# Optimization experiments

Hardware: AMD Instinct MI355X
Metric: run time of the kernel (lower is better)

The kernel has to match this reference:

```python
import jax, jax.numpy as jnp
import numpy as np

B, Hh, Ww, C = 16, 56, 56, 256
NH, WS, SS = 8, 7, 3
HD = C // NH
N = WS * WS
SCALE = HD ** -0.5
EPS = 1e-5


def _rel_pos_index():
    coords = np.stack(np.meshgrid(np.arange(WS), np.arange(WS), indexing='ij'))  # (2, ws, ws)
    cf = coords.reshape(2, -1)
    rc = (cf[:, :, None] - cf[:, None, :]).transpose(1, 2, 0).astype(np.int64)  # (N, N, 2)
    rc[:, :, 0] += WS - 1
    rc[:, :, 1] += WS - 1
    rc[:, :, 0] *= 2 * WS - 1
    return jnp.asarray(rc.sum(-1))  # (N, N)

REL_IDX = _rel_pos_index()


def _shift_mask():
    # standard Swin SW-MSA mask for cyclic shift
    img = np.zeros((1, Hh, Ww, 1), dtype=np.float32)
    cnt = 0
    for hs in (slice(0, -WS), slice(-WS, -SS), slice(-SS, None)):
        for ws_ in (slice(0, -WS), slice(-WS, -SS), slice(-SS, None)):
            img[:, hs, ws_, :] = cnt
            cnt += 1
    mw = img.reshape(1, Hh // WS, WS, Ww // WS, WS, 1).transpose(0, 1, 3, 2, 4, 5).reshape(-1, N)
    am = mw[:, None, :] - mw[:, :, None]
    return jnp.asarray(np.where(am != 0, -100.0, 0.0).astype(np.float32))  # (nW, N, N)


def _ln(x, g, b):
    mu = x.mean(-1, keepdims=True)
    var = ((x - mu) ** 2).mean(-1, keepdims=True)
    return (x - mu) * jax.lax.rsqrt(var + EPS) * g + b


def setup_inputs() -> dict:
    key = jax.random.key(0)
    ks = jax.random.split(key, 8)
    return {
        'x': jax.random.normal(ks[0], (B, Hh * Ww, C), jnp.float32),
        'mask': _shift_mask(),
        'norm1_g': jnp.ones((C,), jnp.float32),
        'norm1_b': jnp.zeros((C,), jnp.float32),
        'qkv_w': jax.random.normal(ks[1], (3 * C, C), jnp.float32) * 0.02,
        'qkv_b': jnp.zeros((3 * C,), jnp.float32),
        'rel_bias': jax.random.normal(ks[2], ((2 * WS - 1) ** 2, NH), jnp.float32) * 0.02,
        'proj_w': jax.random.normal(ks[3], (C, C), jnp.float32) * 0.02,
        'proj_b': jnp.zeros((C,), jnp.float32),
        'norm2_g': jnp.ones((C,), jnp.float32),
        'norm2_b': jnp.zeros((C,), jnp.float32),
        'fc1_w': jax.random.normal(ks[4], (4 * C, C), jnp.float32) * 0.02,
        'fc1_b': jnp.zeros((4 * C,), jnp.float32),
        'fc2_w': jax.random.normal(ks[5], (C, 4 * C), jnp.float32) * 0.02,
        'fc2_b': jnp.zeros((C,), jnp.float32),
    }


def reference(x, mask, norm1_g, norm1_b, qkv_w, qkv_b, rel_bias, proj_w, proj_b,
              norm2_g, norm2_b, fc1_w, fc1_b, fc2_w, fc2_b):
    shortcut = x
    h = _ln(x, norm1_g, norm1_b).reshape(B, Hh, Ww, C)
    # cyclic shift
    h = jnp.roll(h, (-SS, -SS), axis=(1, 2))
    # window partition -> (B*nW, N, C)
    hw = h.reshape(B, Hh // WS, WS, Ww // WS, WS, C).transpose(0, 1, 3, 2, 4, 5).reshape(-1, N, C)
    # qkv projection
    qkv = (hw @ qkv_w.T + qkv_b).reshape(-1, N, 3, NH, HD).transpose(2, 0, 3, 1, 4)
    q, k, v = qkv[0] * SCALE, qkv[1], qkv[2]  # (Bw, NH, N, HD)
    attn = jnp.einsum('bhnd,bhmd->bhnm', q, k)  # (Bw, NH, N, N)
    rpb = rel_bias[REL_IDX.reshape(-1)].reshape(N, N, NH).transpose(2, 0, 1)
    attn = attn + rpb[None]
    nW = mask.shape[0]
    attn = attn.reshape(B, nW, NH, N, N) + mask[None, :, None]
    attn = jax.nn.softmax(attn.reshape(-1, NH, N, N), axis=-1)
    o = jnp.einsum('bhnm,bhmd->bhnd', attn, v).transpose(0, 2, 1, 3).reshape(-1, N, C)
    o = o @ proj_w.T + proj_b
    # window reverse
    o = o.reshape(B, Hh // WS, Ww // WS, WS, WS, C).transpose(0, 1, 3, 2, 4, 5).reshape(B, Hh, Ww, C)
    o = jnp.roll(o, (SS, SS), axis=(1, 2)).reshape(B, Hh * Ww, C)
    x = shortcut + o
    h2 = _ln(x, norm2_g, norm2_b)
    h2 = jax.nn.gelu(h2 @ fc1_w.T + fc1_b, approximate=False)
    return x + (h2 @ fc2_w.T + fc2_b)
```

## Files before the change

kernel.cpp:

```cpp
#include <hip/hip_runtime.h>
#include <cmath>

#define B_    16
#define HH    56
#define WWI   56
#define C_    256
#define NH_   8
#define WS_   7
#define SS_   3
#define HD_   32
#define NTOK  50176
#define NN    49
#define SCALE_ 0.17677669529663689f
#define EPS_  1e-5f

typedef __bf16  bf16x8  __attribute__((ext_vector_type(8)));
typedef float   f32x4   __attribute__((ext_vector_type(4)));
typedef unsigned short ushort8v __attribute__((ext_vector_type(8)));

__device__ __forceinline__ unsigned short f2bf(float f) {
    unsigned int u = __float_as_uint(f);
    unsigned int r = u + 0x7FFFu + ((u >> 16) & 1u);
    return (unsigned short)(r >> 16);
}
__device__ __forceinline__ float bf2f(unsigned short h) {
    return __uint_as_float(((unsigned int)h) << 16);
}
__device__ __forceinline__ float gelu_t(float x) {
    float t = 0.7978845608028654f * (x + 0.044715f * x * x * x);
    float e = __expf(2.0f * t);
    float th = 1.0f - 2.0f * __builtin_amdgcn_rcpf(e + 1.0f);
    return 0.5f * x * (1.0f + th);
}

__device__ __forceinline__ void gload_lds16(const unsigned short* g, unsigned short* l) {
    __builtin_amdgcn_global_load_lds(
        (const __attribute__((address_space(1))) unsigned int*)g,
        (__attribute__((address_space(3))) unsigned int*)l, 16, 0, 0);
}

__global__ __launch_bounds__(256) void convw_k(
    const float* __restrict__ qkvw, const float* __restrict__ projw,
    const float* __restrict__ fc1w, const float* __restrict__ fc2w,
    unsigned short* __restrict__ dst)
{
    int i = blockIdx.x * 256 + threadIdx.x;
    float v;
    if      (i < 196608) v = qkvw[i];
    else if (i < 262144) v = projw[i - 196608];
    else if (i < 524288) v = fc1w[i - 262144];
    else                 v = fc2w[i - 524288];
    dst[i] = f2bf(v);
}

__global__ __launch_bounds__(256) void cb_k(
    const float* __restrict__ mask, const float* __restrict__ relb,
    unsigned short* __restrict__ cb)
{
    int s = blockIdx.x;
    int wi = s >> 3, head = s & 7;
    for (int p = threadIdx.x; p < 2408; p += 256) {
        float v = 0.0f;
        if (p < 2401) {
            int i = p / NN, j = p - i * NN;
            int di = i / 7 - j / 7 + 6, dj = i % 7 - j % 7 + 6;
            v = relb[(di * 13 + dj) * NH_ + head] + mask[(size_t)wi * 2401 + p];
        }
        cb[(size_t)s * 2408 + p] = f2bf(v);
    }
}

__global__ __launch_bounds__(256) void ln_k(
    const float* __restrict__ x, const float* __restrict__ g,
    const float* __restrict__ bta, unsigned short* __restrict__ dst, int shifted)
{
    int wave = threadIdx.x >> 6, lane = threadIdx.x & 63;
    int tok = blockIdx.x * 4 + wave;
    const float4 v = *(const float4*)(x + (size_t)tok * C_ + lane * 4);
    float s = v.x + v.y + v.z + v.w;
    float q = v.x*v.x + v.y*v.y + v.z*v.z + v.w*v.w;
    for (int o = 32; o > 0; o >>= 1) { s += __shfl_xor(s, o, 64); q += __shfl_xor(q, o, 64); }
    float mu  = s * (1.0f / C_);
    float var = q * (1.0f / C_) - mu * mu;
    float rs  = rsqrtf(var + EPS_);
    float4 gg = *(const float4*)(g   + lane * 4);
    float4 bb = *(const float4*)(bta + lane * 4);
    float y0 = (v.x - mu) * rs * gg.x + bb.x;
    float y1 = (v.y - mu) * rs * gg.y + bb.y;
    float y2 = (v.z - mu) * rs * gg.z + bb.z;
    float y3 = (v.w - mu) * rs * gg.w + bb.w;
    size_t di;
    if (shifted) {
        int b = tok / 3136, p = tok % 3136;
        int ph = p / 56, pw = p % 56;
        int sh = ph - SS_; if (sh < 0) sh += HH;
        int sw = pw - SS_; if (sw < 0) sw += WWI;
        int bw = b * 64 + (sh / WS_) * 8 + (sw / WS_);
        int n  = (sh % WS_) * WS_ + (sw % WS_);
        di = ((size_t)bw * NN + n) * C_ + lane * 4;
    } else {
        di = (size_t)tok * C_ + lane * 4;
    }
    unsigned int lo = (unsigned int)f2bf(y0) | ((unsigned int)f2bf(y1) << 16);
    unsigned int hi = (unsigned int)f2bf(y2) | ((unsigned int)f2bf(y3) << 16);
    uint2 u; u.x = lo; u.y = hi;
    *(uint2*)(dst + di) = u;
}

template<int EPI, int NT>
__global__ __launch_bounds__(256) void gemm_k(
    const unsigned short* __restrict__ A, const unsigned short* __restrict__ Bt,
    int K, const float* __restrict__ bias,
    const float* __restrict__ resid, float* __restrict__ outF,
    unsigned short* __restrict__ outQ, unsigned short* __restrict__ outK,
    unsigned short* __restrict__ outV)
{
    __shared__ __align__(16) unsigned char smem[49152];
    const int tid = threadIdx.x;
    const int lin = blockIdx.x;
    const int xcd = lin & 7, t = lin >> 3;
    const int m0 = (xcd * 49 + t / NT) * 128;
    const int n0 = (t % NT) * 128;
    const int wave = tid >> 6, lane = tid & 63, quad = lane >> 4, l16 = lane & 15;
    const int wm = wave >> 1, wn = wave & 1;
    const int r0 = tid >> 2, c0 = (tid & 3) * 8;

    const size_t gA0 = (size_t)(m0 + r0) * K + c0;
    const size_t gA1 = (size_t)(m0 + r0 + 64) * K + c0;
    const size_t gB0 = (size_t)(n0 + r0) * K + c0;
    const size_t gB1 = (size_t)(n0 + r0 + 64) * K + c0;
    const int woff = wave * 512;

    f32x4 acc[4][4] = {};
    const int nk = K >> 5;
    #pragma unroll
    for (int p = 0; p < 2; ++p) {
        unsigned short* sA = (unsigned short*)(smem + p * 16384);
        unsigned short* sB = sA + 4096;
        const int kp = p << 5;
        gload_lds16(A + gA0 + kp, sA + woff);
        gload_lds16(A + gA1 + kp, sA + woff + 2048);
        gload_lds16(Bt + gB0 + kp, sB + woff);
        gload_lds16(Bt + gB1 + kp, sB + woff + 2048);
    }
    int bufc = 0;
    for (int kk = 0; kk < nk; ++kk) {
        if (kk + 2 < nk) {
            int bufn = bufc + 2; if (bufn >= 3) bufn -= 3;
            unsigned short* sA = (unsigned short*)(smem + bufn * 16384);
            unsigned short* sB = sA + 4096;
            const int k2 = (kk + 2) << 5;
            gload_lds16(A + gA0 + k2, sA + woff);
            gload_lds16(A + gA1 + k2, sA + woff + 2048);
            gload_lds16(Bt + gB0 + k2, sB + woff);
            gload_lds16(Bt + gB1 + k2, sB + woff + 2048);
            __asm volatile("s_waitcnt vmcnt(8)\n\ts_barrier" ::: "memory");
        } else if (kk + 1 < nk) {
            __asm volatile("s_waitcnt vmcnt(4)\n\ts_barrier" ::: "memory");
        } else {
            __asm volatile("s_waitcnt vmcnt(0)\n\ts_barrier" ::: "memory");
        }
        const unsigned short* sA = (const unsigned short*)(smem + bufc * 16384);
        const unsigned short* sB = sA + 4096;
        bf16x8 af[4], bfr[4];
        #pragma unroll
        for (int tt = 0; tt < 4; ++tt) {
            af[tt]  = __builtin_bit_cast(bf16x8, *(const ushort8v*)(sA + (wm * 64 + tt * 16 + l16) * 32 + quad * 8));
            bfr[tt] = __builtin_bit_cast(bf16x8, *(const ushort8v*)(sB + (wn * 64 + tt * 16 + l16) * 32 + quad * 8));
        }
        #pragma unroll
        for (int mt = 0; mt < 4; ++mt)
            #pragma unroll
            for (int nt = 0; nt < 4; ++nt)
                acc[mt][nt] = __builtin_amdgcn_mfma_f32_16x16x32_bf16(af[mt], bfr[nt], acc[mt][nt], 0, 0, 0);
        __asm volatile("s_barrier" ::: "memory");
        if (++bufc == 3) bufc = 0;
    }

    float b4[4];
    #pragma unroll
    for (int nt = 0; nt < 4; ++nt) b4[nt] = bias[n0 + wn * 64 + nt * 16 + l16];

    if (EPI == 0 || EPI == 2) {
        unsigned short (*swB)[136] = (unsigned short (*)[136])smem;
        const int seg = n0 >> 8;
        const float qs = (EPI == 0 && seg == 0) ? SCALE_ : 1.0f;
        #pragma unroll
        for (int mt = 0; mt < 4; ++mt)
            #pragma unroll
            for (int nt = 0; nt < 4; ++nt)
                #pragma unroll
                for (int r = 0; r < 4; ++r) {
                    float v = acc[mt][nt][r] + b4[nt];
                    if (EPI == 0) v *= qs; else v = gelu_t(v);
                    swB[wm * 64 + mt * 16 + quad * 4 + r][wn * 64 + nt * 16 + l16] = f2bf(v);
                }
        __syncthreads();
        if (EPI == 0) {
            unsigned short* dstp = seg == 0 ? outQ : (seg == 1 ? outK : outV);
            const int nbase = n0 & 255;
            for (int tt = tid; tt < 2048; tt += 256) {
                int row = tt >> 4, c8 = (tt & 15) * 8;
                int m = m0 + row, bw = m / NN, nw = m - bw * NN;
                int cc = nbase + c8;
                uint4 u = *(uint4*)&swB[row][c8];
                *(uint4*)&dstp[(((size_t)bw * NH_ + (cc >> 5)) * NN + nw) * HD_ + (cc & 31)] = u;
            }
        } else {
            for (int tt = tid; tt < 2048; tt += 256) {
                int row = tt >> 4, c8 = (tt & 15) * 8;
                uint4 u = *(uint4*)&swB[row][c8];
                *(uint4*)&outQ[(size_t)(m0 + row) * 1024 + n0 + c8] = u;
            }
        }
    } else {
        float (*swF)[132] = (float (*)[132])smem;
        #pragma unroll
        for (int p = 0; p < 2; ++p) {
            __syncthreads();
            if (wm == p) {
                #pragma unroll
                for (int mt = 0; mt < 4; ++mt)
                    #pragma unroll
                    for (int nt = 0; nt < 4; ++nt)
                        #pragma unroll
                        for (int r = 0; r < 4; ++r)
                            swF[mt * 16 + quad * 4 + r][wn * 64 + nt * 16 + l16] = acc[mt][nt][r] + b4[nt];
            }
            __syncthreads();
            for (int tt = tid; tt < 2048; tt += 256) {
                int rl = tt >> 5, c4 = (tt & 31) * 4;
                size_t adr;
                if (EPI == 1) {
                    int m = m0 + p * 64 + rl, bw = m / NN, nw = m - bw * NN;
                    int b = bw >> 6, wi = bw & 63;
                    int sh = (wi >> 3) * WS_ + nw / WS_;
                    int sw = (wi & 7) * WS_ + nw % WS_;
                    int ph = sh + SS_; if (ph >= HH)  ph -= HH;
                    int pw = sw + SS_; if (pw >= WWI) pw -= WWI;
                    adr = ((size_t)b * 3136 + ph * 56 + pw) * C_ + n0 + c4;
                } else {
                    adr = (size_t)(m0 + p * 64 + rl) * C_ + n0 + c4;
                }
                float4 u = *(float4*)&swF[rl][c4];
                const float4 rr = (EPI == 1) ? *(const float4*)&resid[adr]
                                             : *(const float4*)&outF[adr];
                u.x += rr.x; u.y += rr.y; u.z += rr.z; u.w += rr.w;
                *(float4*)&outF[adr] = u;
            }
        }
    }
}

__global__ __launch_bounds__(256) void attn_k(
    const unsigned short* __restrict__ qb, const unsigned short* __restrict__ kb,
    const unsigned short* __restrict__ vb, const unsigned short* __restrict__ cb,
    unsigned short* __restrict__ ob)
{
    __shared__ unsigned short qs[64][40];
    __shared__ unsigned short ks[64][40];
    __shared__ unsigned short vt[32][72];
    __shared__ unsigned short sp[64][72];
    __shared__ unsigned short cbs[2408];
    const int tid = threadIdx.x;
    const int bw = blockIdx.x >> 3, head = blockIdx.x & 7;
    const size_t base = (size_t)blockIdx.x * (NN * HD_);

    for (int t = tid; t < 588; t += 256) {
        int seg = t / 196, idx = t - seg * 196;
        int e = idx * 8;
        const unsigned short* src = (seg == 0 ? qb : seg == 1 ? kb : vb) + base + e;
        uint4 u = *(const uint4*)src;
        if (seg == 0)      *(uint4*)&qs[e >> 5][e & 31] = u;
        else if (seg == 1) *(uint4*)&ks[e >> 5][e & 31] = u;
        else {
            int n = e >> 5, hd = e & 31;
            const unsigned short* pu = (const unsigned short*)&u;
            #pragma unroll
            for (int uu = 0; uu < 8; ++uu) vt[hd + uu][n] = pu[uu];
        }
    }
    {
        const unsigned short* cbase = cb + (size_t)(((bw & 63) * 8 + head)) * 2408;
        for (int t = tid; t < 301; t += 256)
            *(uint4*)&cbs[t * 8] = *(const uint4*)(cbase + t * 8);
        for (int t = tid; t < 480; t += 256) vt[t / 15][NN + t % 15] = 0;
    }
    __syncthreads();

    const int wave = tid >> 6, lane = tid & 63, quad = lane >> 4, l16 = lane & 15;
    const f32x4 zz = {};

    bf16x8 afq = __builtin_bit_cast(bf16x8, *(const ushort8v*)&qs[wave * 16 + l16][quad * 8]);
    f32x4 s4[4];
    #pragma unroll
    for (int jt = 0; jt < 4; ++jt) {
        bf16x8 bk = __builtin_bit_cast(bf16x8, *(const ushort8v*)&ks[jt * 16 + l16][quad * 8]);
        s4[jt] = __builtin_amdgcn_mfma_f32_16x16x32_bf16(afq, bk, zz, 0, 0, 0);
    }

    #pragma unroll
    for (int r = 0; r < 4; ++r) {
        int i = wave * 16 + quad * 4 + r;
        float vals[4];
        #pragma unroll
        for (int jt = 0; jt < 4; ++jt) {
            int j = jt * 16 + l16;
            vals[jt] = (i < NN && j < NN) ? s4[jt][r] + bf2f(cbs[i * NN + j]) : -1e30f;
        }
        float mx = fmaxf(fmaxf(vals[0], vals[1]), fmaxf(vals[2], vals[3]));
        #pragma unroll
        for (int o = 1; o < 16; o <<= 1) mx = fmaxf(mx, __shfl_xor(mx, o, 64));
        float e[4], sum = 0.0f;
        #pragma unroll
        for (int jt = 0; jt < 4; ++jt) { e[jt] = __expf(vals[jt] - mx); sum += e[jt]; }
        #pragma unroll
        for (int o = 1; o < 16; o <<= 1) sum += __shfl_xor(sum, o, 64);
        float inv = 1.0f / sum;
        #pragma unroll
        for (int jt = 0; jt < 4; ++jt) sp[i][jt * 16 + l16] = f2bf(e[jt] * inv);
    }
    __syncthreads();

    bf16x8 ap[2];
    #pragma unroll
    for (int kt = 0; kt < 2; ++kt)
        ap[kt] = __builtin_bit_cast(bf16x8, *(const ushort8v*)&sp[wave * 16 + l16][kt * 32 + quad * 8]);
    f32x4 o4[2] = {};
    #pragma unroll
    for (int nt = 0; nt < 2; ++nt)
        #pragma unroll
        for (int kt = 0; kt < 2; ++kt) {
            bf16x8 bv = __builtin_bit_cast(bf16x8, *(const ushort8v*)&vt[nt * 16 + l16][kt * 32 + quad * 8]);
            o4[nt] = __builtin_amdgcn_mfma_f32_16x16x32_bf16(ap[kt], bv, o4[nt], 0, 0, 0);
        }
    #pragma unroll
    for (int nt = 0; nt < 2; ++nt)
        #pragma unroll
        for (int r = 0; r < 4; ++r) {
            int i = wave * 16 + quad * 4 + r;
            if (i < NN)
                ob[((size_t)bw * NN + i) * C_ + head * HD_ + nt * 16 + l16] = f2bf(o4[nt][r]);
        }
}

extern "C" void kernel_launch(void* const* d_in, const int* in_sizes, int n_in,
                              void* d_out, int out_size, void* d_ws, size_t ws_size,
                              hipStream_t stream)
{
    const float* x     = (const float*)d_in[0];
    const float* mask  = (const float*)d_in[1];
    const float* n1g   = (const float*)d_in[2];
    const float* n1b   = (const float*)d_in[3];
    const float* qkvw  = (const float*)d_in[4];
    const float* qkvb  = (const float*)d_in[5];
    const float* relb  = (const float*)d_in[6];
    const float* projw = (const float*)d_in[7];
    const float* projb = (const float*)d_in[8];
    const float* n2g   = (const float*)d_in[9];
    const float* n2b   = (const float*)d_in[10];
    const float* fc1w  = (const float*)d_in[11];
    const float* fc1b  = (const float*)d_in[12];
    const float* fc2w  = (const float*)d_in[13];
    const float* fc2b  = (const float*)d_in[14];
    float* out = (float*)d_out;

    unsigned short* wq = (unsigned short*)d_ws;
    unsigned short* wp = wq + 196608;
    unsigned short* w1 = wq + 262144;
    unsigned short* w2 = wq + 524288;
    unsigned short* hw = wq + 786432;
    unsigned short* qb = hw + 12845056;
    unsigned short* kb = qb + 12845056;
    unsigned short* vb = kb + 12845056;
    unsigned short* ob = vb + 12845056;
    unsigned short* h2 = ob + 12845056;
    unsigned short* a1 = h2 + 12845056;
    unsigned short* cbt = a1;

    convw_k<<<3072, 256, 0, stream>>>(qkvw, projw, fc1w, fc2w, wq);
    cb_k<<<512, 256, 0, stream>>>(mask, relb, cbt);
    ln_k<<<12544, 256, 0, stream>>>(x, n1g, n1b, hw, 1);
    gemm_k<0, 6><<<392 * 6, 256, 0, stream>>>(hw, wq, 256, qkvb, nullptr, nullptr, qb, kb, vb);
    attn_k<<<8192, 256, 0, stream>>>(qb, kb, vb, cbt, ob);
    gemm_k<1, 2><<<392 * 2, 256, 0, stream>>>(ob, wp, 256, projb, x, out, nullptr, nullptr, nullptr);
    ln_k<<<12544, 256, 0, stream>>>(out, n2g, n2b, h2, 0);
    gemm_k<2, 8><<<392 * 8, 256, 0, stream>>>(h2, w1, 256, fc1b, nullptr, nullptr, a1, nullptr, nullptr);
    gemm_k<3, 2><<<392 * 2, 256, 0, stream>>>(a1, w2, 1024, fc2b, nullptr, out, nullptr, nullptr, nullptr);
}
```

Measured before the change: 367.3 us.

## Fuse LayerNorm1, QKV projection and window attention into one per-window kernel

Replaces the LN1, QKV GEMM and attention kernels with a single kernel that handles one shifted window per block. Each block gathers its 49 tokens, normalizes them into LDS, runs the QKV GEMM against streamed weights, and computes all 8 heads' attention on-chip before writing the attention output. This removes the HBM round trips for the normalized activations and for the Q/K/V tensors, plus two kernel launches. The costs are heavy LDS use (about 152KB per block), one block per CU, 1024 blocks that each pad 49 rows up to 64, and reloading the QKV weights in every block.

```diff
diff --git a/kernel.cpp b/kernel.cpp
--- a/kernel.cpp
+++ b/kernel.cpp
@@ -9,7 +9,6 @@
 #define WS_   7
 #define SS_   3
 #define HD_   32
-#define NTOK  50176
 #define NN    49
 #define SCALE_ 0.17677669529663689f
 #define EPS_  1e-5f
@@ -72,7 +71,7 @@
 
 __global__ __launch_bounds__(256) void ln_k(
     const float* __restrict__ x, const float* __restrict__ g,
-    const float* __restrict__ bta, unsigned short* __restrict__ dst, int shifted)
+    const float* __restrict__ bta, unsigned short* __restrict__ dst)
 {
     int wave = threadIdx.x >> 6, lane = threadIdx.x & 63;
     int tok = blockIdx.x * 4 + wave;
@@ -89,22 +88,216 @@
     float y1 = (v.y - mu) * rs * gg.y + bb.y;
     float y2 = (v.z - mu) * rs * gg.z + bb.z;
     float y3 = (v.w - mu) * rs * gg.w + bb.w;
-    size_t di;
-    if (shifted) {
-        int b = tok / 3136, p = tok % 3136;
-        int ph = p / 56, pw = p % 56;
-        int sh = ph - SS_; if (sh < 0) sh += HH;
-        int sw = pw - SS_; if (sw < 0) sw += WWI;
-        int bw = b * 64 + (sh / WS_) * 8 + (sw / WS_);
-        int n  = (sh % WS_) * WS_ + (sw % WS_);
-        di = ((size_t)bw * NN + n) * C_ + lane * 4;
-    } else {
-        di = (size_t)tok * C_ + lane * 4;
-    }
+    size_t di = (size_t)tok * C_ + lane * 4;
     unsigned int lo = (unsigned int)f2bf(y0) | ((unsigned int)f2bf(y1) << 16);
     unsigned int hi = (unsigned int)f2bf(y2) | ((unsigned int)f2bf(y3) << 16);
     uint2 u; u.x = lo; u.y = hi;
     *(uint2*)(dst + di) = u;
+}
+
+#define LK_  0
+#define LQ_  16384
+#define LV_  32768
+#define U1_  49152
+#define U2_  61440
+
+__global__ __launch_bounds__(256, 1) void qkvattn_k(
+    const float* __restrict__ x, const float* __restrict__ n1g,
+    const float* __restrict__ n1b, const unsigned short* __restrict__ qw,
+    const float* __restrict__ qkvb, const unsigned short* __restrict__ cbt,
+    unsigned short* __restrict__ ob)
+{
+    __shared__ __align__(16) unsigned short sm[77824];
+    const int tid = threadIdx.x, bw = blockIdx.x;
+    const int wave = tid >> 6, lane = tid & 63, quad = lane >> 4, l16 = lane & 15;
+    const int b = bw >> 6, wi = bw & 63;
+
+    {
+        const float4 gg = *(const float4*)(n1g + lane * 4);
+        const float4 bb = *(const float4*)(n1b + lane * 4);
+        #pragma unroll
+        for (int g = 0; g < 4; ++g) {
+            float4 vv[4];
+            #pragma unroll
+            for (int j = 0; j < 4; ++j) {
+                int row = wave * 16 + g * 4 + j;
+                if (row < NN) {
+                    int sh_ = (wi >> 3) * WS_ + row / WS_;
+                    int sw_ = (wi & 7) * WS_ + row % WS_;
+                    int ph = sh_ + SS_; if (ph >= HH)  ph -= HH;
+                    int pw = sw_ + SS_; if (pw >= WWI) pw -= WWI;
+                    vv[j] = *(const float4*)(x + ((size_t)b * 3136 + ph * 56 + pw) * C_ + lane * 4);
+                } else { vv[j].x = vv[j].y = vv[j].z = vv[j].w = 0.0f; }
+            }
+            #pragma unroll
+            for (int j = 0; j < 4; ++j) {
+                int row = wave * 16 + g * 4 + j;
+                float4 v = vv[j];
+                float s = v.x + v.y + v.z + v.w;
+                float q2 = v.x*v.x + v.y*v.y + v.z*v.z + v.w*v.w;
+                #pragma unroll
+                for (int o = 32; o > 0; o >>= 1) { s += __shfl_xor(s, o, 64); q2 += __shfl_xor(q2, o, 64); }
+                float mu = s * (1.0f / C_), var = q2 * (1.0f / C_) - mu * mu;
+                float rs = rsqrtf(var + EPS_);
+                float y0 = (v.x - mu) * rs * gg.x + bb.x;
+                float y1 = (v.y - mu) * rs * gg.y + bb.y;
+                float y2 = (v.z - mu) * rs * gg.z + bb.z;
+                float y3 = (v.w - mu) * rs * gg.w + bb.w;
+                if (row >= NN) { y0 = y1 = y2 = y3 = 0.0f; }
+                unsigned int lo = (unsigned int)f2bf(y0) | ((unsigned int)f2bf(y1) << 16);
+                unsigned int hi = (unsigned int)f2bf(y2) | ((unsigned int)f2bf(y3) << 16);
+                uint2 u; u.x = lo; u.y = hi;
+                *(uint2*)&sm[U2_ + (lane >> 3) * 2048 + row * 32 + (lane & 7) * 4] = u;
+            }
+        }
+    }
+    __syncthreads();
+
+    f32x4 aq[6][4][2] = {};
+    {
+        const int r0b = tid >> 2, c0b = (tid & 3) * 8;
+        const int woff = wave * 512;
+        #pragma unroll
+        for (int p = 0; p < 2; ++p) {
+            const unsigned short* src = qw + (size_t)(0 * 128 + r0b) * C_ + p * 32 + c0b;
+            unsigned short* d0 = sm + U1_ + p * 4096 + woff;
+            gload_lds16(src, d0);
+            gload_lds16(src + 64 * C_, d0 + 2048);
+        }
+        #pragma unroll
+        for (int nt6 = 0; nt6 < 6; ++nt6) {
+            #pragma unroll
+            for (int kk = 0; kk < 8; ++kk) {
+                const int it = nt6 * 8 + kk;
+                if (it + 2 < 48) {
+                    const int nt2 = (it + 2) >> 3, kk2 = (it + 2) & 7;
+                    const unsigned short* src = qw + (size_t)(nt2 * 128 + r0b) * C_ + kk2 * 32 + c0b;
+                    unsigned short* d0 = sm + U1_ + ((it + 2) % 3) * 4096 + woff;
+                    gload_lds16(src, d0);
+                    gload_lds16(src + 64 * C_, d0 + 2048);
+                    __asm volatile("s_waitcnt vmcnt(4)\n\ts_barrier" ::: "memory");
+                } else if (it + 1 < 48) {
+                    __asm volatile("s_waitcnt vmcnt(2)\n\ts_barrier" ::: "memory");
+                } else {
+                    __asm volatile("s_waitcnt vmcnt(0)\n\ts_barrier" ::: "memory");
+                }
+                const unsigned short* sB = sm + U1_ + (it % 3) * 4096;
+                const unsigned short* hA = sm + U2_ + kk * 2048;
+                bf16x8 af[4], bf2[2];
+                #pragma unroll
+                for (int mt = 0; mt < 4; ++mt)
+                    af[mt] = __builtin_bit_cast(bf16x8, *(const ushort8v*)(hA + (mt * 16 + l16) * 32 + quad * 8));
+                #pragma unroll
+                for (int nw = 0; nw < 2; ++nw)
+                    bf2[nw] = __builtin_bit_cast(bf16x8, *(const ushort8v*)(sB + (wave * 32 + nw * 16 + l16) * 32 + quad * 8));
+                #pragma unroll
+                for (int mt = 0; mt < 4; ++mt)
+                    #pragma unroll
+                    for (int nw = 0; nw < 2; ++nw)
+                        aq[nt6][mt][nw] = __builtin_amdgcn_mfma_f32_16x16x32_bf16(af[mt], bf2[nw], aq[nt6][mt][nw], 0, 0, 0);
+                __asm volatile("s_barrier" ::: "memory");
+            }
+        }
+    }
+
+    #pragma unroll
+    for (int nt6 = 0; nt6 < 6; ++nt6) {
+        const int seg = nt6 >> 1;
+        #pragma unroll
+        for (int nw = 0; nw < 2; ++nw) {
+            const int n = nt6 * 128 + wave * 32 + nw * 16 + l16;
+            const float bb = qkvb[n];
+            const int nc = n & 255;
+            #pragma unroll
+            for (int mt = 0; mt < 4; ++mt)
+                #pragma unroll
+                for (int r = 0; r < 4; ++r) {
+                    const int m = mt * 16 + quad * 4 + r;
+                    float v = aq[nt6][mt][nw][r] + bb;
+                    int addr;
+                    if (seg == 0)      { v *= SCALE_; addr = LQ_ + (nc >> 5) * 2048 + m * 32 + (nc & 31); }
+                    else if (seg == 1) { addr = LK_ + (nc >> 5) * 2048 + m * 32 + (nc & 31); }
+                    else               { addr = LV_ + (nc >> 5) * 2048 + (m >> 5) * 1024 + (nc & 31) * 32 + (m & 31); }
+                    sm[addr] = f2bf(v);
+                }
+        }
+    }
+    __syncthreads();
+
+    const f32x4 zz = {};
+    unsigned short* cbW = sm + U1_ + wave * 2408;
+    unsigned short* spW = sm + U2_ + wave * 4096;
+    #pragma unroll
+    for (int hh = 0; hh < 2; ++hh) {
+        const int head = wave * 2 + hh;
+        const unsigned short* csrc = cbt + (size_t)(wi * 8 + head) * 2408;
+        for (int t2 = lane; t2 < 301; t2 += 64)
+            *(uint4*)&cbW[t2 * 8] = *(const uint4*)(csrc + t2 * 8);
+        __asm volatile("s_waitcnt vmcnt(0) lgkmcnt(0)" ::: "memory");
+
+        f32x4 s4[4][4];
+        bf16x8 afq[4];
+        #pragma unroll
+        for (int mt = 0; mt < 4; ++mt)
+            afq[mt] = __builtin_bit_cast(bf16x8, *(const ushort8v*)(sm + LQ_ + head * 2048 + (mt * 16 + l16) * 32 + quad * 8));
+        #pragma unroll
+        for (int jt = 0; jt < 4; ++jt) {
+            bf16x8 bk = __builtin_bit_cast(bf16x8, *(const ushort8v*)(sm + LK_ + head * 2048 + (jt * 16 + l16) * 32 + quad * 8));
+            #pragma unroll
+            for (int mt = 0; mt < 4; ++mt)
+                s4[mt][jt] = __builtin_amdgcn_mfma_f32_16x16x32_bf16(afq[mt], bk, zz, 0, 0, 0);
+        }
+        #pragma unroll
+        for (int mt = 0; mt < 4; ++mt)
+            #pragma unroll
+            for (int r = 0; r < 4; ++r) {
+                const int i = mt * 16 + quad * 4 + r;
+                float vals[4];
+                #pragma unroll
+                for (int jt = 0; jt < 4; ++jt) {
+                    const int j = jt * 16 + l16;
+                    vals[jt] = (i < NN && j < NN) ? s4[mt][jt][r] + bf2f(cbW[i * NN + j]) : -1e30f;
+                }
+                float mx = fmaxf(fmaxf(vals[0], vals[1]), fmaxf(vals[2], vals[3]));
+                #pragma unroll
+                for (int o = 1; o < 16; o <<= 1) mx = fmaxf(mx, __shfl_xor(mx, o, 64));
+                float e[4], sum = 0.0f;
+                #pragma unroll
+                for (int jt = 0; jt < 4; ++jt) { e[jt] = __expf(vals[jt] - mx); sum += e[jt]; }
+                #pragma unroll
+                for (int o = 1; o < 16; o <<= 1) sum += __shfl_xor(sum, o, 64);
+                const float inv = 1.0f / sum;
+                #pragma unroll
+                for (int jt = 0; jt < 4; ++jt) {
+                    const int j = jt * 16 + l16;
+                    spW[(j >> 5) * 2048 + i * 32 + (j & 31)] = f2bf(e[jt] * inv);
+                }
+            }
+        __asm volatile("s_waitcnt lgkmcnt(0)" ::: "memory");
+
+        bf16x8 bv[2][2];
+        #pragma unroll
+        for (int nt = 0; nt < 2; ++nt)
+            #pragma unroll
+            for (int kt = 0; kt < 2; ++kt)
+                bv[nt][kt] = __builtin_bit_cast(bf16x8, *(const ushort8v*)(sm + LV_ + head * 2048 + kt * 1024 + (nt * 16 + l16) * 32 + quad * 8));
+        #pragma unroll
+        for (int mt = 0; mt < 4; ++mt) {
+            bf16x8 ap0 = __builtin_bit_cast(bf16x8, *(const ushort8v*)(spW + (mt * 16 + l16) * 32 + quad * 8));
+            bf16x8 ap1 = __builtin_bit_cast(bf16x8, *(const ushort8v*)(spW + 2048 + (mt * 16 + l16) * 32 + quad * 8));
+            #pragma unroll
+            for (int nt = 0; nt < 2; ++nt) {
+                f32x4 o4 = __builtin_amdgcn_mfma_f32_16x16x32_bf16(ap0, bv[nt][0], zz, 0, 0, 0);
+                o4 = __builtin_amdgcn_mfma_f32_16x16x32_bf16(ap1, bv[nt][1], o4, 0, 0, 0);
+                #pragma unroll
+                for (int r = 0; r < 4; ++r) {
+                    const int i = mt * 16 + quad * 4 + r;
+                    if (i < NN)
+                        ob[((size_t)bw * NN + i) * C_ + head * HD_ + nt * 16 + l16] = f2bf(o4[r]);
+                }
+            }
+        }
+    }
 }
 
 template<int EPI, int NT>
@@ -112,8 +305,7 @@
     const unsigned short* __restrict__ A, const unsigned short* __restrict__ Bt,
     int K, const float* __restrict__ bias,
     const float* __restrict__ resid, float* __restrict__ outF,
-    unsigned short* __restrict__ outQ, unsigned short* __restrict__ outK,
-    unsigned short* __restrict__ outV)
+    unsigned short* __restrict__ outQ)
 {
     __shared__ __align__(16) unsigned char smem[49152];
     const int tid = threadIdx.x;
@@ -181,37 +373,21 @@
     #pragma unroll
     for (int nt = 0; nt < 4; ++nt) b4[nt] = bias[n0 + wn * 64 + nt * 16 + l16];
 
-    if (EPI == 0 || EPI == 2) {
+    if (EPI == 2) {
         unsigned short (*swB)[136] = (unsigned short (*)[136])smem;
-        const int seg = n0 >> 8;
-        const float qs = (EPI == 0 && seg == 0) ? SCALE_ : 1.0f;
         #pragma unroll
         for (int mt = 0; mt < 4; ++mt)
             #pragma unroll
             for (int nt = 0; nt < 4; ++nt)
                 #pragma unroll
-                for (int r = 0; r < 4; ++r) {
-                    float v = acc[mt][nt][r] + b4[nt];
-                    if (EPI == 0) v *= qs; else v = gelu_t(v);
-                    swB[wm * 64 + mt * 16 + quad * 4 + r][wn * 64 + nt * 16 + l16] = f2bf(v);
-                }
+                for (int r = 0; r < 4; ++r)
+                    swB[wm * 64 + mt * 16 + quad * 4 + r][wn * 64 + nt * 16 + l16] =
+                        f2bf(gelu_t(acc[mt][nt][r] + b4[nt]));
         __syncthreads();
-        if (EPI == 0) {
-            unsigned short* dstp = seg == 0 ? outQ : (seg == 1 ? outK : outV);
-            const int nbase = n0 & 255;
-            for (int tt = tid; tt < 2048; tt += 256) {
-                int row = tt >> 4, c8 = (tt & 15) * 8;
-                int m = m0 + row, bw = m / NN, nw = m - bw * NN;
-                int cc = nbase + c8;
-                uint4 u = *(uint4*)&swB[row][c8];
-                *(uint4*)&dstp[(((size_t)bw * NH_ + (cc >> 5)) * NN + nw) * HD_ + (cc & 31)] = u;
-            }
-        } else {
-            for (int tt = tid; tt < 2048; tt += 256) {
-                int row = tt >> 4, c8 = (tt & 15) * 8;
-                uint4 u = *(uint4*)&swB[row][c8];
-                *(uint4*)&outQ[(size_t)(m0 + row) * 1024 + n0 + c8] = u;
-            }
+        for (int tt = tid; tt < 2048; tt += 256) {
+            int row = tt >> 4, c8 = (tt & 15) * 8;
+            uint4 u = *(uint4*)&swB[row][c8];
+            *(uint4*)&outQ[(size_t)(m0 + row) * 1024 + n0 + c8] = u;
         }
     } else {
         float (*swF)[132] = (float (*)[132])smem;
@@ -250,98 +426,6 @@
             }
         }
     }
-}
-
-__global__ __launch_bounds__(256) void attn_k(
-    const unsigned short* __restrict__ qb, const unsigned short* __restrict__ kb,
-    const unsigned short* __restrict__ vb, const unsigned short* __restrict__ cb,
-    unsigned short* __restrict__ ob)
-{
-    __shared__ unsigned short qs[64][40];
-    __shared__ unsigned short ks[64][40];
-    __shared__ unsigned short vt[32][72];
-    __shared__ unsigned short sp[64][72];
-    __shared__ unsigned short cbs[2408];
-    const int tid = threadIdx.x;
-    const int bw = blockIdx.x >> 3, head = blockIdx.x & 7;
-    const size_t base = (size_t)blockIdx.x * (NN * HD_);
-
-    for (int t = tid; t < 588; t += 256) {
-        int seg = t / 196, idx = t - seg * 196;
-        int e = idx * 8;
-        const unsigned short* src = (seg == 0 ? qb : seg == 1 ? kb : vb) + base + e;
-        uint4 u = *(const uint4*)src;
-        if (seg == 0)      *(uint4*)&qs[e >> 5][e & 31] = u;
-        else if (seg == 1) *(uint4*)&ks[e >> 5][e & 31] = u;
-        else {
-            int n = e >> 5, hd = e & 31;
-            const unsigned short* pu = (const unsigned short*)&u;
-            #pragma unroll
-            for (int uu = 0; uu < 8; ++uu) vt[hd + uu][n] = pu[uu];
-        }
-    }
-    {
-        const unsigned short* cbase = cb + (size_t)(((bw & 63) * 8 + head)) * 2408;
-        for (int t = tid; t < 301; t += 256)
-            *(uint4*)&cbs[t * 8] = *(const uint4*)(cbase + t * 8);
-        for (int t = tid; t < 480; t += 256) vt[t / 15][NN + t % 15] = 0;
-    }
-    __syncthreads();
-
-    const int wave = tid >> 6, lane = tid & 63, quad = lane >> 4, l16 = lane & 15;
-    const f32x4 zz = {};
-
-    bf16x8 afq = __builtin_bit_cast(bf16x8, *(const ushort8v*)&qs[wave * 16 + l16][quad * 8]);
-    f32x4 s4[4];
-    #pragma unroll
-    for (int jt = 0; jt < 4; ++jt) {
-        bf16x8 bk = __builtin_bit_cast(bf16x8, *(const ushort8v*)&ks[jt * 16 + l16][quad * 8]);
-        s4[jt] = __builtin_amdgcn_mfma_f32_16x16x32_bf16(afq, bk, zz, 0, 0, 0);
-    }
-
-    #pragma unroll
-    for (int r = 0; r < 4; ++r) {
-        int i = wave * 16 + quad * 4 + r;
-        float vals[4];
-        #pragma unroll
-        for (int jt = 0; jt < 4; ++jt) {
-            int j = jt * 16 + l16;
-            vals[jt] = (i < NN && j < NN) ? s4[jt][r] + bf2f(cbs[i * NN + j]) : -1e30f;
-        }
-        float mx = fmaxf(fmaxf(vals[0], vals[1]), fmaxf(vals[2], vals[3]));
-        #pragma unroll
-        for (int o = 1; o < 16; o <<= 1) mx = fmaxf(mx, __shfl_xor(mx, o, 64));
-        float e[4], sum = 0.0f;
-        #pragma unroll
-        for (int jt = 0; jt < 4; ++jt) { e[jt] = __expf(vals[jt] - mx); sum += e[jt]; }
-        #pragma unroll
-        for (int o = 1; o < 16; o <<= 1) sum += __shfl_xor(sum, o, 64);
-        float inv = 1.0f / sum;
-        #pragma unroll
-        for (int jt = 0; jt < 4; ++jt) sp[i][jt * 16 + l16] = f2bf(e[jt] * inv);
-    }
-    __syncthreads();
-
-    bf16x8 ap[2];
-    #pragma unroll
-    for (int kt = 0; kt < 2; ++kt)
-        ap[kt] = __builtin_bit_cast(bf16x8, *(const ushort8v*)&sp[wave * 16 + l16][kt * 32 + quad * 8]);
-    f32x4 o4[2] = {};
-    #pragma unroll
-    for (int nt = 0; nt < 2; ++nt)
-        #pragma unroll
-        for (int kt = 0; kt < 2; ++kt) {
-            bf16x8 bv = __builtin_bit_cast(bf16x8, *(const ushort8v*)&vt[nt * 16 + l16][kt * 32 + quad * 8]);
-            o4[nt] = __builtin_amdgcn_mfma_f32_16x16x32_bf16(ap[kt], bv, o4[nt], 0, 0, 0);
-        }
-    #pragma unroll
-    for (int nt = 0; nt < 2; ++nt)
-        #pragma unroll
-        for (int r = 0; r < 4; ++r) {
-            int i = wave * 16 + quad * 4 + r;
-            if (i < NN)
-                ob[((size_t)bw * NN + i) * C_ + head * HD_ + nt * 16 + l16] = f2bf(o4[nt][r]);
-        }
 }
 
 extern "C" void kernel_launch(void* const* d_in, const int* in_sizes, int n_in,
@@ -369,22 +453,16 @@
     unsigned short* wp = wq + 196608;
     unsigned short* w1 = wq + 262144;
     unsigned short* w2 = wq + 524288;
-    unsigned short* hw = wq + 786432;
-    unsigned short* qb = hw + 12845056;
-    unsigned short* kb = qb + 12845056;
-    unsigned short* vb = kb + 12845056;
-    unsigned short* ob = vb + 12845056;
+    unsigned short* ob = wq + 786432;
     unsigned short* h2 = ob + 12845056;
     unsigned short* a1 = h2 + 12845056;
     unsigned short* cbt = a1;
 
     convw_k<<<3072, 256, 0, stream>>>(qkvw, projw, fc1w, fc2w, wq);
     cb_k<<<512, 256, 0, stream>>>(mask, relb, cbt);
-    ln_k<<<12544, 256, 0, stream>>>(x, n1g, n1b, hw, 1);
-    gemm_k<0, 6><<<392 * 6, 256, 0, stream>>>(hw, wq, 256, qkvb, nullptr, nullptr, qb, kb, vb);
-    attn_k<<<8192, 256, 0, stream>>>(qb, kb, vb, cbt, ob);
-    gemm_k<1, 2><<<392 * 2, 256, 0, stream>>>(ob, wp, 256, projb, x, out, nullptr, nullptr, nullptr);
-    ln_k<<<12544, 256, 0, stream>>>(out, n2g, n2b, h2, 0);
-    gemm_k<2, 8><<<392 * 8, 256, 0, stream>>>(h2, w1, 256, fc1b, nullptr, nullptr, a1, nullptr, nullptr);
-    gemm_k<3, 2><<<392 * 2, 256, 0, stream>>>(a1, w2, 1024, fc2b, nullptr, out, nullptr, nullptr, nullptr);
-}
+    qkvattn_k<<<1024, 256, 0, stream>>>(x, n1g, n1b, wq, qkvb, cbt, ob);
+    gemm_k<1, 2><<<392 * 2, 256, 0, stream>>>(ob, wp, 256, projb, x, out, nullptr);
+    ln_k<<<12544, 256, 0, stream>>>(out, n2g, n2b, h2);
+    gemm_k<2, 8><<<392 * 8, 256, 0, stream>>>(h2, w1, 256, fc1b, nullptr, nullptr, a1);
+    gemm_k<3, 2><<<392 * 2, 256, 0, stream>>>(a1, w2, 1024, fc2b, nullptr, out, nullptr);
+}
```

New measurement: 430.7 us. 1.17x slower.

## Fuse projection GEMM, residual add and second LayerNorm into one kernel

Applied to the files above, without the earlier changes.

Adds a kernel in which each block computes a full 128-row by 256-column strip of the output projection. It then adds bias and the shortcut, writes the fp32 residual, and computes LayerNorm2 in the epilogue, emitting bf16 activations for fc1. This removes the separate LN2 launch and its full reread of the fp32 output. In exchange it launches only 392 blocks with large per-thread accumulators, which lowers occupancy and parallelism for the projection stage.

```diff
diff --git a/kernel.cpp b/kernel.cpp
--- a/kernel.cpp
+++ b/kernel.cpp
@@ -9,7 +9,6 @@
 #define WS_   7
 #define SS_   3
 #define HD_   32
-#define NTOK  50176
 #define NN    49
 #define SCALE_ 0.17677669529663689f
 #define EPS_  1e-5f
@@ -72,7 +71,7 @@
 
 __global__ __launch_bounds__(256) void ln_k(
     const float* __restrict__ x, const float* __restrict__ g,
-    const float* __restrict__ bta, unsigned short* __restrict__ dst, int shifted)
+    const float* __restrict__ bta, unsigned short* __restrict__ dst)
 {
     int wave = threadIdx.x >> 6, lane = threadIdx.x & 63;
     int tok = blockIdx.x * 4 + wave;
@@ -89,18 +88,13 @@
     float y1 = (v.y - mu) * rs * gg.y + bb.y;
     float y2 = (v.z - mu) * rs * gg.z + bb.z;
     float y3 = (v.w - mu) * rs * gg.w + bb.w;
-    size_t di;
-    if (shifted) {
-        int b = tok / 3136, p = tok % 3136;
-        int ph = p / 56, pw = p % 56;
-        int sh = ph - SS_; if (sh < 0) sh += HH;
-        int sw = pw - SS_; if (sw < 0) sw += WWI;
-        int bw = b * 64 + (sh / WS_) * 8 + (sw / WS_);
-        int n  = (sh % WS_) * WS_ + (sw % WS_);
-        di = ((size_t)bw * NN + n) * C_ + lane * 4;
-    } else {
-        di = (size_t)tok * C_ + lane * 4;
-    }
+    int b = tok / 3136, p = tok % 3136;
+    int ph = p / 56, pw = p % 56;
+    int sh = ph - SS_; if (sh < 0) sh += HH;
+    int sw = pw - SS_; if (sw < 0) sw += WWI;
+    int bw = b * 64 + (sh / WS_) * 8 + (sw / WS_);
+    int n  = (sh % WS_) * WS_ + (sw % WS_);
+    size_t di = ((size_t)bw * NN + n) * C_ + lane * 4;
     unsigned int lo = (unsigned int)f2bf(y0) | ((unsigned int)f2bf(y1) << 16);
     unsigned int hi = (unsigned int)f2bf(y2) | ((unsigned int)f2bf(y3) << 16);
     uint2 u; u.x = lo; u.y = hi;
@@ -111,7 +105,7 @@
 __global__ __launch_bounds__(256) void gemm_k(
     const unsigned short* __restrict__ A, const unsigned short* __restrict__ Bt,
     int K, const float* __restrict__ bias,
-    const float* __restrict__ resid, float* __restrict__ outF,
+    float* __restrict__ outF,
     unsigned short* __restrict__ outQ, unsigned short* __restrict__ outK,
     unsigned short* __restrict__ outV)
 {
@@ -230,24 +224,131 @@
             __syncthreads();
             for (int tt = tid; tt < 2048; tt += 256) {
                 int rl = tt >> 5, c4 = (tt & 31) * 4;
-                size_t adr;
-                if (EPI == 1) {
-                    int m = m0 + p * 64 + rl, bw = m / NN, nw = m - bw * NN;
-                    int b = bw >> 6, wi = bw & 63;
-                    int sh = (wi >> 3) * WS_ + nw / WS_;
-                    int sw = (wi & 7) * WS_ + nw % WS_;
-                    int ph = sh + SS_; if (ph >= HH)  ph -= HH;
-                    int pw = sw + SS_; if (pw >= WWI) pw -= WWI;
-                    adr = ((size_t)b * 3136 + ph * 56 + pw) * C_ + n0 + c4;
-                } else {
-                    adr = (size_t)(m0 + p * 64 + rl) * C_ + n0 + c4;
-                }
+                size_t adr = (size_t)(m0 + p * 64 + rl) * C_ + n0 + c4;
                 float4 u = *(float4*)&swF[rl][c4];
-                const float4 rr = (EPI == 1) ? *(const float4*)&resid[adr]
-                                             : *(const float4*)&outF[adr];
+                const float4 rr = *(const float4*)&outF[adr];
                 u.x += rr.x; u.y += rr.y; u.z += rr.z; u.w += rr.w;
                 *(float4*)&outF[adr] = u;
             }
+        }
+    }
+}
+
+__global__ __launch_bounds__(256) void projln_k(
+    const unsigned short* __restrict__ A, const unsigned short* __restrict__ Bt,
+    const float* __restrict__ bias, const float* __restrict__ resid,
+    const float* __restrict__ g2, const float* __restrict__ b2,
+    float* __restrict__ outF, unsigned short* __restrict__ h2)
+{
+    __shared__ __align__(16) unsigned char smem[49152];
+    const int tid = threadIdx.x;
+    const int lin = blockIdx.x;
+    const int xcd = lin & 7, strip = lin >> 3;
+    const int m0 = (xcd * 49 + strip) * 128;
+    const int wave = tid >> 6, lane = tid & 63, quad = lane >> 4, l16 = lane & 15;
+    const int K = C_;
+
+    const int ar = 32 * wave + (lane >> 2), ac = (lane & 3) * 8;
+    const int br = 64 * wave + (lane >> 2);
+
+    f32x4 acc[2][16] = {};
+    {
+        unsigned short* sA = (unsigned short*)smem;
+        unsigned short* sB = sA + 4096;
+        gload_lds16(A + (size_t)(m0 + ar) * K + ac,      sA + wave * 1024);
+        gload_lds16(A + (size_t)(m0 + ar + 16) * K + ac, sA + wave * 1024 + 512);
+        #pragma unroll
+        for (int j = 0; j < 4; ++j)
+            gload_lds16(Bt + (size_t)(br + 16 * j) * K + ac, sB + wave * 2048 + j * 512);
+    }
+    for (int kk = 0; kk < 8; ++kk) {
+        if (kk + 1 < 8) {
+            unsigned short* sA = (unsigned short*)(smem + ((kk + 1) & 1) * 24576);
+            unsigned short* sB = sA + 4096;
+            const int k1 = (kk + 1) << 5;
+            gload_lds16(A + (size_t)(m0 + ar) * K + k1 + ac,      sA + wave * 1024);
+            gload_lds16(A + (size_t)(m0 + ar + 16) * K + k1 + ac, sA + wave * 1024 + 512);
+            #pragma unroll
+            for (int j = 0; j < 4; ++j)
+                gload_lds16(Bt + (size_t)(br + 16 * j) * K + k1 + ac, sB + wave * 2048 + j * 512);
+            __asm volatile("s_waitcnt vmcnt(6)\n\ts_barrier" ::: "memory");
+        } else {
+            __asm volatile("s_waitcnt vmcnt(0)\n\ts_barrier" ::: "memory");
+        }
+        const unsigned short* sA = (const unsigned short*)(smem + (kk & 1) * 24576);
+        const unsigned short* sB = sA + 4096;
+        bf16x8 af[2];
+        #pragma unroll
+        for (int mt = 0; mt < 2; ++mt)
+            af[mt] = __builtin_bit_cast(bf16x8, *(const ushort8v*)(sA + (wave * 32 + mt * 16 + l16) * 32 + quad * 8));
+        #pragma unroll
+        for (int nt = 0; nt < 16; ++nt) {
+            bf16x8 bfr = __builtin_bit_cast(bf16x8, *(const ushort8v*)(sB + (nt * 16 + l16) * 32 + quad * 8));
+            #pragma unroll
+            for (int mt = 0; mt < 2; ++mt)
+                acc[mt][nt] = __builtin_amdgcn_mfma_f32_16x16x32_bf16(af[mt], bfr, acc[mt][nt], 0, 0, 0);
+        }
+        __asm volatile("s_barrier" ::: "memory");
+    }
+
+    float b16v[16];
+    #pragma unroll
+    for (int nt = 0; nt < 16; ++nt) b16v[nt] = bias[nt * 16 + l16];
+
+    float* fbuf = (float*)smem;
+    const int j = tid & 7, rloc = tid >> 3;
+    #pragma unroll
+    for (int p = 0; p < 4; ++p) {
+        __syncthreads();
+        if (wave == p) {
+            #pragma unroll
+            for (int mt = 0; mt < 2; ++mt)
+                #pragma unroll
+                for (int nt = 0; nt < 16; ++nt)
+                    #pragma unroll
+                    for (int r = 0; r < 4; ++r)
+                        fbuf[(mt * 16 + quad * 4 + r) * 260 + nt * 16 + l16] = acc[mt][nt][r] + b16v[nt];
+        }
+        __syncthreads();
+        const int m = m0 + p * 32 + rloc;
+        const int bw = m / NN, nw = m - bw * NN;
+        const int b_ = bw >> 6, wi = bw & 63;
+        const int sh = (wi >> 3) * WS_ + nw / WS_;
+        const int sw = (wi & 7) * WS_ + nw % WS_;
+        int ph = sh + SS_; if (ph >= HH)  ph -= HH;
+        int pw = sw + SS_; if (pw >= WWI) pw -= WWI;
+        const size_t base = ((size_t)b_ * 3136 + ph * 56 + pw) * C_;
+        float4 v[8]; float sum = 0.0f, sq = 0.0f;
+        #pragma unroll
+        for (int q = 0; q < 8; ++q) {
+            const int qq = (q + j) & 7;
+            const int ch = j * 32 + qq * 4;
+            float4 a4 = *(float4*)&fbuf[rloc * 260 + ch];
+            const float4 r4 = *(const float4*)&resid[base + ch];
+            a4.x += r4.x; a4.y += r4.y; a4.z += r4.z; a4.w += r4.w;
+            *(float4*)&outF[base + ch] = a4;
+            sum += a4.x + a4.y + a4.z + a4.w;
+            sq  += a4.x*a4.x + a4.y*a4.y + a4.z*a4.z + a4.w*a4.w;
+            v[qq] = a4;
+        }
+        #pragma unroll
+        for (int o = 1; o < 8; o <<= 1) { sum += __shfl_xor(sum, o, 64); sq += __shfl_xor(sq, o, 64); }
+        const float mu = sum * (1.0f / C_);
+        const float var = sq * (1.0f / C_) - mu * mu;
+        const float rs = rsqrtf(var + EPS_);
+        #pragma unroll
+        for (int q = 0; q < 8; ++q) {
+            const int ch = j * 32 + q * 4;
+            const float4 g4  = *(const float4*)&g2[ch];
+            const float4 bb4 = *(const float4*)&b2[ch];
+            float y0 = (v[q].x - mu) * rs * g4.x + bb4.x;
+            float y1 = (v[q].y - mu) * rs * g4.y + bb4.y;
+            float y2 = (v[q].z - mu) * rs * g4.z + bb4.z;
+            float y3 = (v[q].w - mu) * rs * g4.w + bb4.w;
+            uint2 u;
+            u.x = (unsigned int)f2bf(y0) | ((unsigned int)f2bf(y1) << 16);
+            u.y = (unsigned int)f2bf(y2) | ((unsigned int)f2bf(y3) << 16);
+            *(uint2*)&h2[base + ch] = u;
         }
     }
 }
@@ -305,8 +406,8 @@
         float vals[4];
         #pragma unroll
         for (int jt = 0; jt < 4; ++jt) {
-            int j = jt * 16 + l16;
-            vals[jt] = (i < NN && j < NN) ? s4[jt][r] + bf2f(cbs[i * NN + j]) : -1e30f;
+            int jx = jt * 16 + l16;
+            vals[jt] = (i < NN && jx < NN) ? s4[jt][r] + bf2f(cbs[i * NN + jx]) : -1e30f;
         }
         float mx = fmaxf(fmaxf(vals[0], vals[1]), fmaxf(vals[2], vals[3]));
         #pragma unroll
@@ -380,11 +481,10 @@
 
     convw_k<<<3072, 256, 0, stream>>>(qkvw, projw, fc1w, fc2w, wq);
     cb_k<<<512, 256, 0, stream>>>(mask, relb, cbt);
-    ln_k<<<12544, 256, 0, stream>>>(x, n1g, n1b, hw, 1);
-    gemm_k<0, 6><<<392 * 6, 256, 0, stream>>>(hw, wq, 256, qkvb, nullptr, nullptr, qb, kb, vb);
+    ln_k<<<12544, 256, 0, stream>>>(x, n1g, n1b, hw);
+    gemm_k<0, 6><<<392 * 6, 256, 0, stream>>>(hw, wq, 256, qkvb, nullptr, qb, kb, vb);
     attn_k<<<8192, 256, 0, stream>>>(qb, kb, vb, cbt, ob);
-    gemm_k<1, 2><<<392 * 2, 256, 0, stream>>>(ob, wp, 256, projb, x, out, nullptr, nullptr, nullptr);
-    ln_k<<<12544, 256, 0, stream>>>(out, n2g, n2b, h2, 0);
-    gemm_k<2, 8><<<392 * 8, 256, 0, stream>>>(h2, w1, 256, fc1b, nullptr, nullptr, a1, nullptr, nullptr);
-    gemm_k<3, 2><<<392 * 2, 256, 0, stream>>>(a1, w2, 1024, fc2b, nullptr, out, nullptr, nullptr, nullptr);
-}
+    projln_k<<<392, 256, 0, stream>>>(ob, wp, projb, x, n2g, n2b, out, h2);
+    gemm_k<2, 8><<<392 * 8, 256, 0, stream>>>(h2, w1, 256, fc1b, nullptr, a1, nullptr, nullptr);
+    gemm_k<3, 2><<<392 * 2, 256, 0, stream>>>(a1, w2, 1024, fc2b, out, nullptr, nullptr, nullptr);
+}
```

After: 472.2 us. 28.5% more time.
